# Optimization experiments

Measured on AMD Instinct MI355X. Metric: run time of the kernel, lower is better.

Reference implementation:

```python
import jax, jax.numpy as jnp
import numpy as np

HEADS = 8
DIM_HEAD = 64
SCALE = DIM_HEAD ** -0.5
QUERY_DIM = 512
CTX_DIM = 64
INNER = HEADS * DIM_HEAD  # 512
GATE_HID = 32


def setup_inputs() -> dict:
    key = jax.random.key(0)
    ks = jax.random.split(key, 11)
    B, N, M = 4, 2048, 2048
    s = lambda fan: 1.0 / np.sqrt(fan)
    return {
        "x": jax.random.normal(ks[0], (B, N, QUERY_DIM), dtype=jnp.float32),
        "context": jax.random.normal(ks[1], (B, M, CTX_DIM), dtype=jnp.float32),
        "Wq": jax.random.normal(ks[2], (QUERY_DIM, INNER), dtype=jnp.float32) * s(QUERY_DIM),
        "Wk": jax.random.normal(ks[3], (CTX_DIM, INNER), dtype=jnp.float32) * s(CTX_DIM),
        "Wv": jax.random.normal(ks[4], (CTX_DIM, INNER), dtype=jnp.float32) * s(CTX_DIM),
        "W1": jax.random.normal(ks[5], (CTX_DIM, GATE_HID), dtype=jnp.float32) * s(CTX_DIM),
        "b1": jnp.zeros((GATE_HID,), dtype=jnp.float32),
        "W2": jax.random.normal(ks[6], (GATE_HID, 1), dtype=jnp.float32) * s(GATE_HID),
        "b2": jnp.zeros((1,), dtype=jnp.float32),
        "Wo": jax.random.normal(ks[7], (INNER, QUERY_DIM), dtype=jnp.float32) * s(INNER),
        "bo": jnp.zeros((QUERY_DIM,), dtype=jnp.float32),
    }


def reference(x, context, Wq, Wk, Wv, W1, b1, W2, b2, Wo, bo):
    B, N, _ = x.shape
    M = context.shape[1]
    # visual reliability gate: sigmoid(relu(ctx @ W1 + b1) @ W2 + b2) -> [B, M, 1]
    gate = jax.nn.sigmoid(jax.nn.relu(context @ W1 + b1) @ W2 + b2)
    ctx = context * gate
    # projections
    q = (x @ Wq).reshape(B, N, HEADS, DIM_HEAD).transpose(0, 2, 1, 3)    # [B,H,N,D]
    k = (ctx @ Wk).reshape(B, M, HEADS, DIM_HEAD).transpose(0, 2, 1, 3)  # [B,H,M,D]
    v = (ctx @ Wv).reshape(B, M, HEADS, DIM_HEAD).transpose(0, 2, 1, 3)  # [B,H,M,D]
    # scaled dot-product attention (full score matrix, as in source)
    sim = jnp.einsum('bhid,bhjd->bhij', q, k) * SCALE
    attn = jax.nn.softmax(sim, axis=-1)
    out = jnp.einsum('bhij,bhjd->bhid', attn, v)
    out = out.transpose(0, 2, 1, 3).reshape(B, N, INNER)
    return out @ Wo + bo
```

## Files before the change

kernel.cpp:

```cpp
#include <hip/hip_runtime.h>

typedef unsigned short u16;
typedef unsigned int u32;
using frag16 = __attribute__((ext_vector_type(8))) short;
using facc   = __attribute__((ext_vector_type(4))) float;
using facc16 = __attribute__((ext_vector_type(16))) float;

#define DEV static __device__ __forceinline__

DEV u16 f2bf(float f) {
  union { float f; unsigned u; } v; v.f = f;
  unsigned r = v.u + 0x7fffu + ((v.u >> 16) & 1u);
  return (u16)(r >> 16);
}
DEV unsigned fbits(float f) {
  union { float f; unsigned u; } v; v.f = f;
  return v.u;
}
DEV unsigned pkbf(float lo, float hi) {
  return __builtin_amdgcn_perm(fbits(hi) + 0x8000u, fbits(lo) + 0x8000u, 0x07060302u);
}
DEV void gld16(const u16* g, u16* l) {
  __builtin_amdgcn_global_load_lds(
      (__attribute__((address_space(1))) unsigned int*)(g),
      (__attribute__((address_space(3))) unsigned int*)(l), 16, 0, 0);
}

__global__ __launch_bounds__(256) void prep_kernel(const float4* __restrict__ x,
    const float* __restrict__ Wq, const float* __restrict__ Wk,
    const float* __restrict__ Wv, const float* __restrict__ Wo,
    u16* __restrict__ xb, u16* __restrict__ WqT, u16* __restrict__ WkT,
    u16* __restrict__ WvT, u16* __restrict__ WoT) {
  int bid = blockIdx.x;
  if (bid < 4096) {
    int id = bid * 256 + threadIdx.x;
    float4 v = x[id];
    ushort4 o;
    o.x = f2bf(v.x); o.y = f2bf(v.y); o.z = f2bf(v.z); o.w = f2bf(v.w);
    *(ushort4*)(xb + (size_t)id * 4) = o;
  } else {
    int id = (bid - 4096) * 256 + threadIdx.x;
    const float* W; u16* WT; int K, idx;
    if (id < 262144)      { W = Wq; WT = WqT; K = 512; idx = id; }
    else if (id < 294912) { W = Wk; WT = WkT; K = 64;  idx = id - 262144; }
    else if (id < 327680) { W = Wv; WT = WvT; K = 64;  idx = id - 294912; }
    else                  { W = Wo; WT = WoT; K = 512; idx = id - 327680; }
    int n = idx / K, k = idx - n * K;
    WT[idx] = f2bf(W[k * 512 + n]);
  }
}

__global__ __launch_bounds__(256) void gate_kernel(const float* __restrict__ ctx,
    const float* __restrict__ W1, const float* __restrict__ b1,
    const float* __restrict__ W2, const float* __restrict__ b2,
    u16* __restrict__ gctx) {
  int wave = threadIdx.x >> 6, lane = threadIdx.x & 63;
  int row = blockIdx.x * 4 + wave;
  __shared__ float sc[4][64];
  float cv = ctx[(size_t)row * 64 + lane];
  sc[wave][lane] = cv;
  __syncthreads();
  float h = 0.f;
  if (lane < 32) {
    h = b1[lane];
    #pragma unroll
    for (int i = 0; i < 64; ++i) h += sc[wave][i] * W1[i * 32 + lane];
    h = fmaxf(h, 0.f) * W2[lane];
  }
  #pragma unroll
  for (int off = 32; off; off >>= 1) h += __shfl_xor(h, off);
  float g = 1.f / (1.f + __expf(-(h + b2[0])));
  gctx[(size_t)row * 64 + lane] = f2bf(cv * g);
}

template<int MODE>
__global__ __launch_bounds__(256) void gemm128(const u16* __restrict__ A,
    const u16* __restrict__ BT, void* __restrict__ Cp,
    const float* __restrict__ bias, int N, float scale) {
  const int K = 512;
  const int lane = threadIdx.x & 63, wave = threadIdx.x >> 6;
  const int quad = lane >> 4, l16 = lane & 15;
  const int wr = wave >> 1, wc = wave & 1;
  const int m0 = blockIdx.y * 128, n0 = blockIdx.x * 64;

  __shared__ __align__(16) u16 As[2][128 * 32];
  __shared__ __align__(16) u16 Bs[2][64 * 32];

  const u16* gA = A + (size_t)(m0 + wave * 32 + (lane >> 2)) * K + (lane & 3) * 8;
  const u16* gB = BT + (size_t)(n0 + wave * 16 + (lane >> 2)) * K + (lane & 3) * 8;

  facc acc[4][2] = {};

  for (int k0 = 0; k0 < K; k0 += 64) {
    if (k0) __syncthreads();
    gld16(gA + k0,           As[0] + wave * 1024);
    gld16(gA + 16 * K + k0,  As[0] + wave * 1024 + 512);
    gld16(gA + k0 + 32,          As[1] + wave * 1024);
    gld16(gA + 16 * K + k0 + 32, As[1] + wave * 1024 + 512);
    gld16(gB + k0,      Bs[0] + wave * 512);
    gld16(gB + k0 + 32, Bs[1] + wave * 512);
    __syncthreads();

    #pragma unroll
    for (int hh = 0; hh < 2; ++hh) {
      frag16 af[4], bf[2];
      #pragma unroll
      for (int rt = 0; rt < 4; ++rt)
        af[rt] = *(const frag16*)(As[hh] + (wr * 64 + rt * 16 + l16) * 32 + quad * 8);
      #pragma unroll
      for (int ct = 0; ct < 2; ++ct)
        bf[ct] = *(const frag16*)(Bs[hh] + (wc * 32 + ct * 16 + l16) * 32 + quad * 8);
      #pragma unroll
      for (int rt = 0; rt < 4; ++rt)
        #pragma unroll
        for (int ct = 0; ct < 2; ++ct)
          acc[rt][ct] = __builtin_amdgcn_mfma_f32_16x16x32_bf16(af[rt], bf[ct], acc[rt][ct], 0, 0, 0);
    }
  }

  #pragma unroll
  for (int rt = 0; rt < 4; ++rt) {
    #pragma unroll
    for (int ct = 0; ct < 2; ++ct) {
      int col = n0 + wc * 32 + ct * 16 + l16;
      int r0g = m0 + wr * 64 + rt * 16 + quad * 4;
      if (MODE == 0) {
        u16* C = (u16*)Cp;
        #pragma unroll
        for (int r = 0; r < 4; ++r)
          C[(size_t)(r0g + r) * N + col] = f2bf(acc[rt][ct][r] * scale);
      } else {
        float* C = (float*)Cp;
        float bv = bias[col];
        #pragma unroll
        for (int r = 0; r < 4; ++r)
          C[(size_t)(r0g + r) * N + col] = acc[rt][ct][r] + bv;
      }
    }
  }
}

__global__ __launch_bounds__(256) void gemm_kv(const u16* __restrict__ A,
    const u16* __restrict__ BkT, const u16* __restrict__ BvT,
    u16* __restrict__ Kp, u16* __restrict__ Vp) {
  const int Kd = 64, N = 512;
  int lane = threadIdx.x & 63, wave = threadIdx.x >> 6;
  int quad = lane >> 4, l16 = lane & 15;
  int wr = wave >> 1, wc = wave & 1;
  int rowBase = blockIdx.y * 64 + wr * 32;
  int colBase = blockIdx.x * 64 + wc * 32;
  facc ak[2][2] = {}, av[2][2] = {};
  const u16* a0 = A + (size_t)(rowBase + l16) * Kd + quad * 8;
  const u16* a1 = a0 + (size_t)16 * Kd;
  const u16* bk0 = BkT + (size_t)(colBase + l16) * Kd + quad * 8;
  const u16* bk1 = bk0 + (size_t)16 * Kd;
  const u16* bv0 = BvT + (size_t)(colBase + l16) * Kd + quad * 8;
  const u16* bv1 = bv0 + (size_t)16 * Kd;
  #pragma unroll
  for (int kk = 0; kk < Kd; kk += 32) {
    frag16 af0 = *(const frag16*)(a0 + kk);
    frag16 af1 = *(const frag16*)(a1 + kk);
    frag16 k0 = *(const frag16*)(bk0 + kk);
    frag16 k1 = *(const frag16*)(bk1 + kk);
    frag16 v0 = *(const frag16*)(bv0 + kk);
    frag16 v1 = *(const frag16*)(bv1 + kk);
    ak[0][0] = __builtin_amdgcn_mfma_f32_16x16x32_bf16(af0, k0, ak[0][0], 0, 0, 0);
    ak[0][1] = __builtin_amdgcn_mfma_f32_16x16x32_bf16(af0, k1, ak[0][1], 0, 0, 0);
    ak[1][0] = __builtin_amdgcn_mfma_f32_16x16x32_bf16(af1, k0, ak[1][0], 0, 0, 0);
    ak[1][1] = __builtin_amdgcn_mfma_f32_16x16x32_bf16(af1, k1, ak[1][1], 0, 0, 0);
    av[0][0] = __builtin_amdgcn_mfma_f32_16x16x32_bf16(af0, v0, av[0][0], 0, 0, 0);
    av[0][1] = __builtin_amdgcn_mfma_f32_16x16x32_bf16(af0, v1, av[0][1], 0, 0, 0);
    av[1][0] = __builtin_amdgcn_mfma_f32_16x16x32_bf16(af1, v0, av[1][0], 0, 0, 0);
    av[1][1] = __builtin_amdgcn_mfma_f32_16x16x32_bf16(af1, v1, av[1][1], 0, 0, 0);
  }
  #pragma unroll
  for (int rt = 0; rt < 2; ++rt) {
    #pragma unroll
    for (int ct = 0; ct < 2; ++ct) {
      int col = colBase + ct * 16 + l16;
      int r0g = rowBase + rt * 16 + quad * 4;
      int hh = col >> 6, d = col & 63;
      int b = r0g >> 11;
      #pragma unroll
      for (int r = 0; r < 4; ++r) {
        int m = (r0g + r) & 2047;
        size_t addr = ((((size_t)(b * 8 + hh) * 64 + (m >> 5)) * 4 + (d >> 4)) * 64
                       + ((d >> 3) & 1) * 32 + (m & 31)) * 8 + (d & 7);
        Kp[addr] = f2bf(ak[rt][ct][r]);
      }
      int m = r0g & 2047;
      size_t addr = ((((size_t)(b * 8 + hh) * 64 + (m >> 5)) * 4
                      + ((m >> 4) & 1) * 2 + (d >> 5)) * 64
                     + ((m >> 3) & 1) * 32 + (d & 31)) * 8 + (m & 7);
      ushort4 o;
      o.x = f2bf(av[rt][ct][0]); o.y = f2bf(av[rt][ct][1]);
      o.z = f2bf(av[rt][ct][2]); o.w = f2bf(av[rt][ct][3]);
      *(ushort4*)(Vp + addr) = o;
    }
  }
}

__global__ __launch_bounds__(256, 3) void attn_kernel(
    const u16* __restrict__ qb, const u16* __restrict__ Kp,
    const u16* __restrict__ Vp, float* __restrict__ Opart,
    float* __restrict__ Lpart) {
  const int lane = threadIdx.x & 63, wave = threadIdx.x >> 6;
  const int l32 = lane & 31;
  const int hi = lane >> 5;
  const int bid = blockIdx.x;
  const int bh = bid & 31;
  const int qblk = (bid >> 5) & 15;
  const int js = bid >> 9;
  const int b = bh >> 3, h = bh & 7;
  const int q0 = (qblk * 4 + wave) * 32;
  const int rowg = b * 2048 + q0 + l32;

  const u16* qp = qb + (size_t)rowg * 512 + h * 64 + hi * 8;
  frag16 qf0 = *(const frag16*)(qp);
  frag16 qf1 = *(const frag16*)(qp + 16);
  frag16 qf2 = *(const frag16*)(qp + 32);
  frag16 qf3 = *(const frag16*)(qp + 48);

  facc16 O0 = {}, O1 = {};
  float lsum = 0.f;

  const size_t ts = 2048;
  const u16* kpb = Kp + (size_t)(bh * 64 + js * 32) * ts + lane * 8;
  const u16* vpb = Vp + (size_t)(bh * 64 + js * 32) * ts + lane * 8;

  frag16 kf[4], vf[4];
  #pragma unroll
  for (int i = 0; i < 4; ++i) {
    kf[i] = *(const frag16*)(kpb + i * 512);
    vf[i] = *(const frag16*)(vpb + i * 512);
  }

  for (int t = 0; t < 32; ++t) {
    int tn = (t < 31) ? t + 1 : 31;
    const u16* ktn = kpb + (size_t)tn * ts;
    const u16* vtn = vpb + (size_t)tn * ts;
    frag16 nkf[4], nvf[4];
    #pragma unroll
    for (int i = 0; i < 4; ++i) {
      nkf[i] = *(const frag16*)(ktn + i * 512);
      nvf[i] = *(const frag16*)(vtn + i * 512);
    }

    facc16 S = {};
    S = __builtin_amdgcn_mfma_f32_32x32x16_bf16(kf[0], qf0, S, 0, 0, 0);
    S = __builtin_amdgcn_mfma_f32_32x32x16_bf16(kf[1], qf1, S, 0, 0, 0);
    S = __builtin_amdgcn_mfma_f32_32x32x16_bf16(kf[2], qf2, S, 0, 0, 0);
    S = __builtin_amdgcn_mfma_f32_32x32x16_bf16(kf[3], qf3, S, 0, 0, 0);

    float e[16];
    #pragma unroll
    for (int r = 0; r < 16; ++r) e[r] = __builtin_amdgcn_exp2f(S[r]);
    #pragma unroll
    for (int r = 0; r < 16; ++r) lsum += e[r];

    unsigned pu[2][4];
    #pragma unroll
    for (int c = 0; c < 2; ++c) {
      const float* ee = e + c * 8;
      unsigned L0 = pkbf(ee[0], ee[1]);
      unsigned L1 = pkbf(ee[2], ee[3]);
      unsigned H0 = pkbf(ee[4], ee[5]);
      unsigned H1 = pkbf(ee[6], ee[7]);
      unsigned Y0 = hi ? L0 : H0;
      unsigned Y1 = hi ? L1 : H1;
      unsigned X0 = (unsigned)__shfl_xor((int)Y0, 32);
      unsigned X1 = (unsigned)__shfl_xor((int)Y1, 32);
      pu[c][0] = hi ? X0 : L0;
      pu[c][1] = hi ? X1 : L1;
      pu[c][2] = hi ? H0 : X0;
      pu[c][3] = hi ? H1 : X1;
    }
    frag16 P0 = *(frag16*)&pu[0][0];
    frag16 P1 = *(frag16*)&pu[1][0];

    O0 = __builtin_amdgcn_mfma_f32_32x32x16_bf16(vf[0], P0, O0, 0, 0, 0);
    O0 = __builtin_amdgcn_mfma_f32_32x32x16_bf16(vf[2], P1, O0, 0, 0, 0);
    O1 = __builtin_amdgcn_mfma_f32_32x32x16_bf16(vf[1], P0, O1, 0, 0, 0);
    O1 = __builtin_amdgcn_mfma_f32_32x32x16_bf16(vf[3], P1, O1, 0, 0, 0);

    #pragma unroll
    for (int i = 0; i < 4; ++i) { kf[i] = nkf[i]; vf[i] = nvf[i]; }
  }

  lsum += __shfl_xor(lsum, 32);

  float* op = Opart + ((size_t)js * 8192 + rowg) * 512 + h * 64;
  #pragma unroll
  for (int dt = 0; dt < 2; ++dt) {
    #pragma unroll
    for (int rq = 0; rq < 4; ++rq) {
      float4 v;
      if (dt == 0) { v.x = O0[rq*4]; v.y = O0[rq*4+1]; v.z = O0[rq*4+2]; v.w = O0[rq*4+3]; }
      else         { v.x = O1[rq*4]; v.y = O1[rq*4+1]; v.z = O1[rq*4+2]; v.w = O1[rq*4+3]; }
      int d0 = dt * 32 + 8 * rq + 4 * hi;
      *(float4*)(op + d0) = v;
    }
  }
  if (!hi) Lpart[(size_t)js * 65536 + (size_t)rowg * 8 + h] = lsum;
}

__global__ __launch_bounds__(256) void combine_kernel(const float* __restrict__ Opart,
    const float* __restrict__ Lpart, u16* __restrict__ ob) {
  int id = blockIdx.x * 256 + threadIdx.x;
  int row = id >> 7, c4 = (id & 127) * 4;
  int hh = c4 >> 6;
  size_t o = (size_t)row * 512 + c4;
  const float4 o0 = *(const float4*)(Opart + o);
  const float4 o1 = *(const float4*)(Opart + (size_t)8192 * 512 + o);
  float rl = 1.f / (Lpart[(size_t)row * 8 + hh] + Lpart[65536 + (size_t)row * 8 + hh]);
  ushort4 u;
  u.x = f2bf((o0.x + o1.x) * rl);
  u.y = f2bf((o0.y + o1.y) * rl);
  u.z = f2bf((o0.z + o1.z) * rl);
  u.w = f2bf((o0.w + o1.w) * rl);
  *(ushort4*)(ob + o) = u;
}

extern "C" void kernel_launch(void* const* d_in, const int* in_sizes, int n_in,
                              void* d_out, int out_size, void* d_ws, size_t ws_size,
                              hipStream_t stream) {
  const float* x   = (const float*)d_in[0];
  const float* ctx = (const float*)d_in[1];
  const float* Wq  = (const float*)d_in[2];
  const float* Wk  = (const float*)d_in[3];
  const float* Wv  = (const float*)d_in[4];
  const float* W1  = (const float*)d_in[5];
  const float* b1  = (const float*)d_in[6];
  const float* W2  = (const float*)d_in[7];
  const float* b2  = (const float*)d_in[8];
  const float* Wo  = (const float*)d_in[9];
  const float* bo  = (const float*)d_in[10];
  float* out = (float*)d_out;

  char* ws = (char*)d_ws;
  size_t off = 0;
  auto alloc = [&](size_t bytes) {
    char* p = ws + off;
    off += (bytes + 255) & ~(size_t)255;
    return p;
  };
  u16* xb    = (u16*)alloc(8192ull * 512 * 2);
  u16* qb    = (u16*)alloc(8192ull * 512 * 2);
  u16* Kp    = (u16*)alloc(8192ull * 512 * 2);
  u16* Vp    = (u16*)alloc(8192ull * 512 * 2);
  u16* ob    = (u16*)alloc(8192ull * 512 * 2);
  u16* gctx  = (u16*)alloc(8192ull * 64 * 2);
  u16* WqT   = (u16*)alloc(512ull * 512 * 2);
  u16* WkT   = (u16*)alloc(512ull * 64 * 2);
  u16* WvT   = (u16*)alloc(512ull * 64 * 2);
  u16* WoT   = (u16*)alloc(512ull * 512 * 2);
  float* Opart = (float*)alloc(2ull * 8192 * 512 * 4);
  float* Lpart = (float*)alloc(2ull * 65536 * 4);

  prep_kernel<<<6400, 256, 0, stream>>>((const float4*)x, Wq, Wk, Wv, Wo,
                                        xb, WqT, WkT, WvT, WoT);
  gate_kernel<<<2048, 256, 0, stream>>>(ctx, W1, b1, W2, b2, gctx);

  gemm128<0><<<dim3(8, 64), 256, 0, stream>>>(xb, WqT, qb, nullptr, 512,
                                              0.125f * 1.4426950408889634f);
  gemm_kv<<<dim3(8, 128), 256, 0, stream>>>(gctx, WkT, WvT, Kp, Vp);

  attn_kernel<<<1024, 256, 0, stream>>>(qb, Kp, Vp, Opart, Lpart);
  combine_kernel<<<4096, 256, 0, stream>>>(Opart, Lpart, ob);

  gemm128<2><<<dim3(8, 64), 256, 0, stream>>>(ob, WoT, out, bo, 512, 1.f);
}
```

Before: 186.7 us.

## Merge prep/gate and Q/KV projection launches; double-buffer K/V prefetch in attention

Folds the gate computation into the prep kernel and the Q projection and KV projection GEMMs into one kernel dispatched by block index, cutting the launch count from seven to five and letting independent work share the GPU. The attention loop now keeps two K/V tile register sets and prefetches two tiles ahead instead of one, to hide global load latency. This raises VGPR pressure in the attention kernel and may lower occupancy. The fused projection kernel also reserves the GEMM's shared memory for the KV blocks, which never use it.

```diff
diff --git a/kernel.cpp b/kernel.cpp
--- a/kernel.cpp
+++ b/kernel.cpp
@@ -26,11 +26,14 @@
       (__attribute__((address_space(3))) unsigned int*)(l), 16, 0, 0);
 }
 
-__global__ __launch_bounds__(256) void prep_kernel(const float4* __restrict__ x,
+__global__ __launch_bounds__(256) void prep_gate_kernel(const float4* __restrict__ x,
     const float* __restrict__ Wq, const float* __restrict__ Wk,
     const float* __restrict__ Wv, const float* __restrict__ Wo,
+    const float* __restrict__ ctx, const float* __restrict__ W1,
+    const float* __restrict__ b1, const float* __restrict__ W2,
+    const float* __restrict__ b2,
     u16* __restrict__ xb, u16* __restrict__ WqT, u16* __restrict__ WkT,
-    u16* __restrict__ WvT, u16* __restrict__ WoT) {
+    u16* __restrict__ WvT, u16* __restrict__ WoT, u16* __restrict__ gctx) {
   int bid = blockIdx.x;
   if (bid < 4096) {
     int id = bid * 256 + threadIdx.x;
@@ -38,7 +41,7 @@
     ushort4 o;
     o.x = f2bf(v.x); o.y = f2bf(v.y); o.z = f2bf(v.z); o.w = f2bf(v.w);
     *(ushort4*)(xb + (size_t)id * 4) = o;
-  } else {
+  } else if (bid < 6400) {
     int id = (bid - 4096) * 256 + threadIdx.x;
     const float* W; u16* WT; int K, idx;
     if (id < 262144)      { W = Wq; WT = WqT; K = 512; idx = id; }
@@ -47,44 +50,36 @@
     else                  { W = Wo; WT = WoT; K = 512; idx = id - 327680; }
     int n = idx / K, k = idx - n * K;
     WT[idx] = f2bf(W[k * 512 + n]);
-  }
-}
-
-__global__ __launch_bounds__(256) void gate_kernel(const float* __restrict__ ctx,
-    const float* __restrict__ W1, const float* __restrict__ b1,
-    const float* __restrict__ W2, const float* __restrict__ b2,
-    u16* __restrict__ gctx) {
-  int wave = threadIdx.x >> 6, lane = threadIdx.x & 63;
-  int row = blockIdx.x * 4 + wave;
-  __shared__ float sc[4][64];
-  float cv = ctx[(size_t)row * 64 + lane];
-  sc[wave][lane] = cv;
-  __syncthreads();
-  float h = 0.f;
-  if (lane < 32) {
-    h = b1[lane];
-    #pragma unroll
-    for (int i = 0; i < 64; ++i) h += sc[wave][i] * W1[i * 32 + lane];
-    h = fmaxf(h, 0.f) * W2[lane];
-  }
-  #pragma unroll
-  for (int off = 32; off; off >>= 1) h += __shfl_xor(h, off);
-  float g = 1.f / (1.f + __expf(-(h + b2[0])));
-  gctx[(size_t)row * 64 + lane] = f2bf(cv * g);
+  } else {
+    int wave = threadIdx.x >> 6, lane = threadIdx.x & 63;
+    int row = (bid - 6400) * 4 + wave;
+    __shared__ float sc[4][64];
+    float cv = ctx[(size_t)row * 64 + lane];
+    sc[wave][lane] = cv;
+    __syncthreads();
+    float h = 0.f;
+    if (lane < 32) {
+      h = b1[lane];
+      #pragma unroll
+      for (int i = 0; i < 64; ++i) h += sc[wave][i] * W1[i * 32 + lane];
+      h = fmaxf(h, 0.f) * W2[lane];
+    }
+    #pragma unroll
+    for (int off = 32; off; off >>= 1) h += __shfl_xor(h, off);
+    float g = 1.f / (1.f + __expf(-(h + b2[0])));
+    gctx[(size_t)row * 64 + lane] = f2bf(cv * g);
+  }
 }
 
 template<int MODE>
-__global__ __launch_bounds__(256) void gemm128(const u16* __restrict__ A,
-    const u16* __restrict__ BT, void* __restrict__ Cp,
-    const float* __restrict__ bias, int N, float scale) {
-  const int K = 512;
+DEV void gemm128_body(const u16* __restrict__ A, const u16* __restrict__ BT,
+                      void* __restrict__ Cp, const float* __restrict__ bias,
+                      int m0, int n0, float scale,
+                      u16* As0, u16* As1, u16* Bs0, u16* Bs1) {
+  const int K = 512, N = 512;
   const int lane = threadIdx.x & 63, wave = threadIdx.x >> 6;
   const int quad = lane >> 4, l16 = lane & 15;
   const int wr = wave >> 1, wc = wave & 1;
-  const int m0 = blockIdx.y * 128, n0 = blockIdx.x * 64;
-
-  __shared__ __align__(16) u16 As[2][128 * 32];
-  __shared__ __align__(16) u16 Bs[2][64 * 32];
 
   const u16* gA = A + (size_t)(m0 + wave * 32 + (lane >> 2)) * K + (lane & 3) * 8;
   const u16* gB = BT + (size_t)(n0 + wave * 16 + (lane >> 2)) * K + (lane & 3) * 8;
@@ -93,23 +88,25 @@
 
   for (int k0 = 0; k0 < K; k0 += 64) {
     if (k0) __syncthreads();
-    gld16(gA + k0,           As[0] + wave * 1024);
-    gld16(gA + 16 * K + k0,  As[0] + wave * 1024 + 512);
-    gld16(gA + k0 + 32,          As[1] + wave * 1024);
-    gld16(gA + 16 * K + k0 + 32, As[1] + wave * 1024 + 512);
-    gld16(gB + k0,      Bs[0] + wave * 512);
-    gld16(gB + k0 + 32, Bs[1] + wave * 512);
+    gld16(gA + k0,           As0 + wave * 1024);
+    gld16(gA + 16 * K + k0,  As0 + wave * 1024 + 512);
+    gld16(gA + k0 + 32,          As1 + wave * 1024);
+    gld16(gA + 16 * K + k0 + 32, As1 + wave * 1024 + 512);
+    gld16(gB + k0,      Bs0 + wave * 512);
+    gld16(gB + k0 + 32, Bs1 + wave * 512);
     __syncthreads();
 
     #pragma unroll
     for (int hh = 0; hh < 2; ++hh) {
+      const u16* Ah = hh ? As1 : As0;
+      const u16* Bh = hh ? Bs1 : Bs0;
       frag16 af[4], bf[2];
       #pragma unroll
       for (int rt = 0; rt < 4; ++rt)
-        af[rt] = *(const frag16*)(As[hh] + (wr * 64 + rt * 16 + l16) * 32 + quad * 8);
+        af[rt] = *(const frag16*)(Ah + (wr * 64 + rt * 16 + l16) * 32 + quad * 8);
       #pragma unroll
       for (int ct = 0; ct < 2; ++ct)
-        bf[ct] = *(const frag16*)(Bs[hh] + (wc * 32 + ct * 16 + l16) * 32 + quad * 8);
+        bf[ct] = *(const frag16*)(Bh + (wc * 32 + ct * 16 + l16) * 32 + quad * 8);
       #pragma unroll
       for (int rt = 0; rt < 4; ++rt)
         #pragma unroll
@@ -140,17 +137,28 @@
   }
 }
 
-__global__ __launch_bounds__(256) void gemm_kv(const u16* __restrict__ A,
-    const u16* __restrict__ BkT, const u16* __restrict__ BvT,
-    u16* __restrict__ Kp, u16* __restrict__ Vp) {
-  const int Kd = 64, N = 512;
+__global__ __launch_bounds__(256) void proj_kernel(const u16* __restrict__ xb,
+    const u16* __restrict__ WqT, u16* __restrict__ qb,
+    const u16* __restrict__ gctx, const u16* __restrict__ BkT,
+    const u16* __restrict__ BvT, u16* __restrict__ Kp, u16* __restrict__ Vp) {
+  __shared__ __align__(16) u16 As0[128 * 32], As1[128 * 32];
+  __shared__ __align__(16) u16 Bs0[64 * 32], Bs1[64 * 32];
+  int bid = blockIdx.x;
+  if (bid < 512) {
+    int n0 = (bid & 7) * 64, m0 = (bid >> 3) * 128;
+    gemm128_body<0>(xb, WqT, qb, nullptr, m0, n0,
+                    0.125f * 1.4426950408889634f, As0, As1, Bs0, Bs1);
+    return;
+  }
+  bid -= 512;
+  const int Kd = 64;
   int lane = threadIdx.x & 63, wave = threadIdx.x >> 6;
   int quad = lane >> 4, l16 = lane & 15;
   int wr = wave >> 1, wc = wave & 1;
-  int rowBase = blockIdx.y * 64 + wr * 32;
-  int colBase = blockIdx.x * 64 + wc * 32;
+  int rowBase = (bid >> 3) * 64 + wr * 32;
+  int colBase = (bid & 7) * 64 + wc * 32;
   facc ak[2][2] = {}, av[2][2] = {};
-  const u16* a0 = A + (size_t)(rowBase + l16) * Kd + quad * 8;
+  const u16* a0 = gctx + (size_t)(rowBase + l16) * Kd + quad * 8;
   const u16* a1 = a0 + (size_t)16 * Kd;
   const u16* bk0 = BkT + (size_t)(colBase + l16) * Kd + quad * 8;
   const u16* bk1 = bk0 + (size_t)16 * Kd;
@@ -228,36 +236,26 @@
   const u16* kpb = Kp + (size_t)(bh * 64 + js * 32) * ts + lane * 8;
   const u16* vpb = Vp + (size_t)(bh * 64 + js * 32) * ts + lane * 8;
 
-  frag16 kf[4], vf[4];
+  frag16 kA[4], vA[4], kB[4], vB[4];
   #pragma unroll
   for (int i = 0; i < 4; ++i) {
-    kf[i] = *(const frag16*)(kpb + i * 512);
-    vf[i] = *(const frag16*)(vpb + i * 512);
-  }
-
-  for (int t = 0; t < 32; ++t) {
-    int tn = (t < 31) ? t + 1 : 31;
-    const u16* ktn = kpb + (size_t)tn * ts;
-    const u16* vtn = vpb + (size_t)tn * ts;
-    frag16 nkf[4], nvf[4];
-    #pragma unroll
-    for (int i = 0; i < 4; ++i) {
-      nkf[i] = *(const frag16*)(ktn + i * 512);
-      nvf[i] = *(const frag16*)(vtn + i * 512);
-    }
-
+    kA[i] = *(const frag16*)(kpb + i * 512);
+    vA[i] = *(const frag16*)(vpb + i * 512);
+    kB[i] = *(const frag16*)(kpb + ts + i * 512);
+    vB[i] = *(const frag16*)(vpb + ts + i * 512);
+  }
+
+  auto computeTile = [&](frag16* kf, frag16* vf) {
     facc16 S = {};
     S = __builtin_amdgcn_mfma_f32_32x32x16_bf16(kf[0], qf0, S, 0, 0, 0);
     S = __builtin_amdgcn_mfma_f32_32x32x16_bf16(kf[1], qf1, S, 0, 0, 0);
     S = __builtin_amdgcn_mfma_f32_32x32x16_bf16(kf[2], qf2, S, 0, 0, 0);
     S = __builtin_amdgcn_mfma_f32_32x32x16_bf16(kf[3], qf3, S, 0, 0, 0);
-
     float e[16];
     #pragma unroll
     for (int r = 0; r < 16; ++r) e[r] = __builtin_amdgcn_exp2f(S[r]);
     #pragma unroll
     for (int r = 0; r < 16; ++r) lsum += e[r];
-
     unsigned pu[2][4];
     #pragma unroll
     for (int c = 0; c < 2; ++c) {
@@ -277,14 +275,35 @@
     }
     frag16 P0 = *(frag16*)&pu[0][0];
     frag16 P1 = *(frag16*)&pu[1][0];
-
     O0 = __builtin_amdgcn_mfma_f32_32x32x16_bf16(vf[0], P0, O0, 0, 0, 0);
     O0 = __builtin_amdgcn_mfma_f32_32x32x16_bf16(vf[2], P1, O0, 0, 0, 0);
     O1 = __builtin_amdgcn_mfma_f32_32x32x16_bf16(vf[1], P0, O1, 0, 0, 0);
     O1 = __builtin_amdgcn_mfma_f32_32x32x16_bf16(vf[3], P1, O1, 0, 0, 0);
-
-    #pragma unroll
-    for (int i = 0; i < 4; ++i) { kf[i] = nkf[i]; vf[i] = nvf[i]; }
+  };
+
+  for (int t = 0; t < 32; t += 2) {
+    computeTile(kA, vA);
+    {
+      int tn = (t + 2 < 32) ? t + 2 : 31;
+      const u16* kt = kpb + (size_t)tn * ts;
+      const u16* vt = vpb + (size_t)tn * ts;
+      #pragma unroll
+      for (int i = 0; i < 4; ++i) {
+        kA[i] = *(const frag16*)(kt + i * 512);
+        vA[i] = *(const frag16*)(vt + i * 512);
+      }
+    }
+    computeTile(kB, vB);
+    {
+      int tn = (t + 3 < 32) ? t + 3 : 31;
+      const u16* kt = kpb + (size_t)tn * ts;
+      const u16* vt = vpb + (size_t)tn * ts;
+      #pragma unroll
+      for (int i = 0; i < 4; ++i) {
+        kB[i] = *(const frag16*)(kt + i * 512);
+        vB[i] = *(const frag16*)(vt + i * 512);
+      }
+    }
   }
 
   lsum += __shfl_xor(lsum, 32);
@@ -319,6 +338,15 @@
   u.z = f2bf((o0.z + o1.z) * rl);
   u.w = f2bf((o0.w + o1.w) * rl);
   *(ushort4*)(ob + o) = u;
+}
+
+__global__ __launch_bounds__(256) void gemm_out(const u16* __restrict__ A,
+    const u16* __restrict__ BT, float* __restrict__ C,
+    const float* __restrict__ bias) {
+  __shared__ __align__(16) u16 As0[128 * 32], As1[128 * 32];
+  __shared__ __align__(16) u16 Bs0[64 * 32], Bs1[64 * 32];
+  int n0 = (blockIdx.x & 7) * 64, m0 = (blockIdx.x >> 3) * 128;
+  gemm128_body<2>(A, BT, C, bias, m0, n0, 1.f, As0, As1, Bs0, Bs1);
 }
 
 extern "C" void kernel_launch(void* const* d_in, const int* in_sizes, int n_in,
@@ -357,16 +385,11 @@
   float* Opart = (float*)alloc(2ull * 8192 * 512 * 4);
   float* Lpart = (float*)alloc(2ull * 65536 * 4);
 
-  prep_kernel<<<6400, 256, 0, stream>>>((const float4*)x, Wq, Wk, Wv, Wo,
-                                        xb, WqT, WkT, WvT, WoT);
-  gate_kernel<<<2048, 256, 0, stream>>>(ctx, W1, b1, W2, b2, gctx);
-
-  gemm128<0><<<dim3(8, 64), 256, 0, stream>>>(xb, WqT, qb, nullptr, 512,
-                                              0.125f * 1.4426950408889634f);
-  gemm_kv<<<dim3(8, 128), 256, 0, stream>>>(gctx, WkT, WvT, Kp, Vp);
-
+  prep_gate_kernel<<<8448, 256, 0, stream>>>((const float4*)x, Wq, Wk, Wv, Wo,
+                                             ctx, W1, b1, W2, b2,
+                                             xb, WqT, WkT, WvT, WoT, gctx);
+  proj_kernel<<<1536, 256, 0, stream>>>(xb, WqT, qb, gctx, WkT, WvT, Kp, Vp);
   attn_kernel<<<1024, 256, 0, stream>>>(qb, Kp, Vp, Opart, Lpart);
   combine_kernel<<<4096, 256, 0, stream>>>(Opart, Lpart, ob);
-
-  gemm128<2><<<dim3(8, 64), 256, 0, stream>>>(ob, WoT, out, bo, 512, 1.f);
-}
+  gemm_out<<<512, 256, 0, stream>>>(ob, WoT, out, bo);
+}
```

Result: no change. 187.3 us (+0.3%).
